# Performance work log

Hardware: AMD Instinct MI355X
Metric: run time of the kernel (lower is better)

Reference implementation:

```python
import jax, jax.numpy as jnp
import numpy as np

B, S, D, H, DFF = 4, 2048, 512, 8, 2048
HD = D // H  # head dim = 64
LN_EPS = 1e-5


def setup_inputs() -> dict:
    key = jax.random.key(0)
    ks = jax.random.split(key, 12)
    sc = 0.02
    return {
        "x": jax.random.normal(ks[0], (B, S, D), jnp.float32),
        "Wq": jax.random.normal(ks[1], (D, D), jnp.float32) * sc,
        "bq": jnp.zeros((D,), jnp.float32),
        "Wk": jax.random.normal(ks[2], (D, D), jnp.float32) * sc,
        "bk": jnp.zeros((D,), jnp.float32),
        "Wv": jax.random.normal(ks[3], (D, D), jnp.float32) * sc,
        "bv": jnp.zeros((D,), jnp.float32),
        "W1": jax.random.normal(ks[4], (D, DFF), jnp.float32) * sc,
        "b1": jnp.zeros((DFF,), jnp.float32),
        "W2": jax.random.normal(ks[5], (DFF, D), jnp.float32) * sc,
        "b2": jnp.zeros((D,), jnp.float32),
        "gamma": jnp.ones((D,), jnp.float32),
        "beta": jnp.zeros((D,), jnp.float32),
    }


def reference(x, Wq, bq, Wk, bk, Wv, bv, W1, b1, W2, b2, gamma, beta):
    # Multi-head self-attention (explicit bmm -> softmax -> bmm chain)
    q = (x @ Wq + bq).reshape(B, S, H, HD)
    k = (x @ Wk + bk).reshape(B, S, H, HD)
    v = (x @ Wv + bv).reshape(B, S, H, HD)
    scores = jnp.einsum("bqhd,bkhd->bhqk", q, k) / jnp.sqrt(jnp.float32(HD))
    atn = jax.nn.softmax(scores, axis=-1)          # [B,H,S,S]
    attn_out = jnp.einsum("bhqk,bkhd->bqhd", atn, v).reshape(B, S, D)
    # FFN with residual + LayerNorm (residual around FFN only, as in source)
    h = jax.nn.relu(attn_out @ W1 + b1)
    y = h @ W2 + b2 + attn_out
    mu = jnp.mean(y, axis=-1, keepdims=True)
    var = jnp.var(y, axis=-1, keepdims=True)
    out = (y - mu) * jax.lax.rsqrt(var + LN_EPS) * gamma + beta
    return (out, atn)
```

## Files before the change

kernel.cpp:

```cpp
#include <hip/hip_runtime.h>
#include <hip/hip_bf16.h>

#define TPB 256
typedef long long ll;


using short8  = __attribute__((ext_vector_type(8))) short;
using short4v = __attribute__((ext_vector_type(4))) short;
using floatx4 = __attribute__((ext_vector_type(4))) float;

__device__ __forceinline__ unsigned short f2bu(float f) {
    union { float f; unsigned int u; } v; v.f = f;
    unsigned int u = v.u;
    return (unsigned short)((u + 0x7fffu + ((u >> 16) & 1u)) >> 16);
}

__device__ __forceinline__ float bu2f(unsigned short us) {
    union { unsigned int u; float f; } v; v.u = ((unsigned int)us) << 16;
    return v.f;
}

__device__ __forceinline__ unsigned int cvtpk(float lo, float hi) {
    unsigned int r;
    asm volatile("v_cvt_pk_bf16_f32 %0, %1, %2" : "=v"(r) : "v"(lo), "v"(hi));
    return r;
}

__device__ __forceinline__ float fexp2(float x) {
#if __has_builtin(__builtin_amdgcn_exp2f)
    return __builtin_amdgcn_exp2f(x);
#else
    float r;
    asm("v_exp_f32 %0, %1" : "=v"(r) : "v"(x));
    return r;
#endif
}

__device__ __forceinline__ floatx4 mfma16(short4v a, short4v b, floatx4 c) {
#if __has_builtin(__builtin_amdgcn_mfma_f32_16x16x16bf16_1k)
    return __builtin_amdgcn_mfma_f32_16x16x16bf16_1k(a, b, c, 0, 0, 0);
#else
    floatx4 d;
    asm volatile("v_mfma_f32_16x16x16_bf16 %0, %1, %2, %3"
                 : "=v"(d) : "v"(a), "v"(b), "v"(c));
    return d;
#endif
}

__device__ __forceinline__ void gload16(const unsigned short* g, unsigned short* l) {
    __builtin_amdgcn_global_load_lds(
        (const __attribute__((address_space(1))) void*)g,
        (__attribute__((address_space(3))) void*)l, 16, 0, 0);
}

#define QSCALE 0.18033688f

template<int BM, int BN, int EPI>
__device__ __forceinline__ void gemm_body(
    const unsigned short* __restrict__ Ap, const unsigned short* __restrict__ BTp,
    const float* __restrict__ bias, void* __restrict__ Cp,
    const unsigned short* __restrict__ Rb, unsigned short* __restrict__ Vtp,
    int K, ll lda, ll ldb, ll ldc, int bx, int by,
    unsigned short* Asm, unsigned short* Bsm)
{
    constexpr int BK = 64;
    const int tid  = threadIdx.x;
    const int lane = tid & 63;
    const int wave = tid >> 6;
    const int wm = wave >> 1, wn = wave & 1;
    constexpr int WM = BM / 2, WN = BN / 2, FM = WM / 16, FN = WN / 16;

    const ll brow = (ll)bx * BM;
    const ll bcol = (ll)by * BN;
    const int srow = lane >> 3;
    const int ssw  = (((lane & 7) ^ srow)) << 3;
    const int kswz = (lane & 7) << 3;

    floatx4 acc[FM][FN] = {};

    for (int k0 = 0; k0 < K; k0 += BK) {
        #pragma unroll
        for (int ii = 0; ii < BM / 32; ++ii) {
            int i = wave + ii * 4;
            gload16(Ap + (brow + i * 8 + srow) * lda + k0 + ssw, Asm + i * 512);
        }
        #pragma unroll
        for (int ii = 0; ii < BN / 32; ++ii) {
            int i = wave + ii * 4;
            gload16(BTp + (bcol + i * 8 + srow) * ldb + k0 + ssw, Bsm + i * 512);
        }
        __syncthreads();

        #pragma unroll
        for (int kk = 0; kk < BK; kk += 32) {
            short8 af[FM], bfr[FN];
            const int kidx = (kk + ((lane >> 4) << 3)) ^ kswz;
            const int ar = wm * WM + (lane & 15);
            const int bc = wn * WN + (lane & 15);
            #pragma unroll
            for (int m = 0; m < FM; m++)
                af[m] = *(const short8*)&Asm[(ar + m * 16) * BK + kidx];
            #pragma unroll
            for (int n = 0; n < FN; n++)
                bfr[n] = *(const short8*)&Bsm[(bc + n * 16) * BK + kidx];
            #pragma unroll
            for (int m = 0; m < FM; m++)
                #pragma unroll
                for (int n = 0; n < FN; n++)
                    acc[m][n] = __builtin_amdgcn_mfma_f32_16x16x32_bf16(af[m], bfr[n], acc[m][n], 0, 0, 0);
        }
        __syncthreads();
    }

    const ll crow0 = brow + wm * WM + ((lane >> 4) << 2);
    const ll ccol0 = bcol + wn * WN + (lane & 15);

    if constexpr (EPI == 7) {
        if (ccol0 >= 1024) {
            const int bz = (int)(brow >> 11);
            #pragma unroll
            for (int m = 0; m < FM; m++) {
                const int sl = (int)((crow0 + m * 16) & 2047);
                #pragma unroll
                for (int n = 0; n < FN; n++) {
                    const int col = (int)(ccol0 + n * 16);
                    const float bv = bias[col];
                    const int hdg = col - 1024;
                    unsigned int u0 = cvtpk(acc[m][n][0] + bv, acc[m][n][1] + bv);
                    unsigned int u1 = cvtpk(acc[m][n][2] + bv, acc[m][n][3] + bv);
                    int2 t = { (int)u0, (int)u1 };
                    *(int2*)(Vtp + ((ll)((bz * 8 + (hdg >> 6)) * 64 + (hdg & 63))) * 2048 + sl) = t;
                }
            }
            return;
        }
    }

    #pragma unroll
    for (int m = 0; m < FM; m++) {
        #pragma unroll
        for (int j = 0; j < 4; j++) {
            ll row = crow0 + m * 16 + j;
            #pragma unroll
            for (int np = 0; np < FN; np += 2) {
                ll col0 = ccol0 + np * 16;
                ll col1 = col0 + 16;
                float v0 = acc[m][np][j]     + bias[col0];
                float v1 = acc[m][np + 1][j] + bias[col1];
                if constexpr (EPI == 3) {
                    v0 = v0 > 0.f ? v0 : 0.f;
                    v1 = v1 > 0.f ? v1 : 0.f;
                } else if constexpr (EPI == 6) {
                    v0 += bu2f(Rb[row * ldc + col0]);
                    v1 += bu2f(Rb[row * ldc + col1]);
                } else if constexpr (EPI == 7) {
                    if (col0 < 512) v0 *= QSCALE;
                    if (col1 < 512) v1 *= QSCALE;
                }
                unsigned int r = cvtpk(v0, v1);
                ((unsigned short*)Cp)[row * ldc + col0] = (unsigned short)r;
                ((unsigned short*)Cp)[row * ldc + col1] = (unsigned short)(r >> 16);
            }
        }
    }
}

template<int BM, int BN, int EPI>
__global__ __launch_bounds__(TPB) void gemm_k(
    const unsigned short* __restrict__ Ap, const unsigned short* __restrict__ BTp,
    const float* __restrict__ bias, void* __restrict__ Cp,
    const unsigned short* __restrict__ Rb, unsigned short* __restrict__ Vtp,
    int K, ll lda, ll ldb, ll ldc)
{
    __shared__ unsigned short sh[BM * 64 + BN * 64];
    int nwg = gridDim.x * gridDim.y;
    int sid = blockIdx.y * gridDim.x + blockIdx.x;
    int cpx = nwg >> 3;
    int w = (sid & 7) * cpx + (sid >> 3);
    int bx = w % gridDim.x, by = w / gridDim.x;
    gemm_body<BM, BN, EPI>(Ap, BTp, bias, Cp, Rb, Vtp, K, lda, ldb, ldc, bx, by,
                           sh, sh + BM * 64);
}

__device__ __forceinline__ void atnwrite_body(
    const unsigned short* __restrict__ qkv, const float* __restrict__ ilbuf,
    float* __restrict__ atn, int bh, int qt, unsigned short* sh)
{
    unsigned short* Qsm = sh;
    unsigned short* Ksm = sh + 8192;
    float* Pst = (float*)sh;

    const int tid = threadIdx.x, lane = tid & 63, wave = tid >> 6;
    const int c0 = lane & 15, g = lane >> 4;
    const int b = bh >> 3, h = bh & 7;

    const ll qbase  = ((ll)(b * 2048 + qt * 128)) * 1536 + h * 64;
    const ll kbase0 = ((ll)(b * 2048)) * 1536 + 512 + h * 64;
    const int srow = lane >> 3;
    const int ssw  = (((lane & 7) ^ srow)) << 3;
    const int kswz = (lane & 7) << 3;

    #pragma unroll
    for (int ii = 0; ii < 4; ++ii) {
        int i = wave + ii * 4;
        gload16(qkv + qbase + (ll)(i * 8 + srow) * 1536 + ssw, Qsm + i * 512);
    }
    __syncthreads();
    short8 qf[2][2];
    #pragma unroll
    for (int nq = 0; nq < 2; nq++)
        #pragma unroll
        for (int kk = 0; kk < 2; kk++)
            qf[nq][kk] = *(const short8*)&Qsm[(wave * 32 + nq * 16 + c0) * 64 + ((kk * 32 + g * 8) ^ kswz)];

    float il2[2];
    #pragma unroll
    for (int nq = 0; nq < 2; nq++)
        il2[nq] = ilbuf[(ll)bh * 2048 + qt * 128 + wave * 32 + nq * 16 + c0];

    float* myP = Pst + wave * 1024;

    for (int kb = 0; kb < 16; ++kb) {
        const ll koff = kbase0 + (ll)kb * 128 * 1536;
        #pragma unroll
        for (int ii = 0; ii < 4; ++ii) {
            int i = wave + ii * 4;
            gload16(qkv + koff + (ll)(i * 8 + srow) * 1536 + ssw, Ksm + i * 512);
        }
        __syncthreads();

        floatx4 sacc[8][2] = {};
        #pragma unroll
        for (int kk = 0; kk < 2; kk++)
            #pragma unroll
            for (int mk = 0; mk < 8; mk++) {
                short8 kf = *(const short8*)&Ksm[(mk * 16 + c0) * 64 + ((kk * 32 + g * 8) ^ kswz)];
                #pragma unroll
                for (int nq = 0; nq < 2; nq++)
                    sacc[mk][nq] = __builtin_amdgcn_mfma_f32_16x16x32_bf16(kf, qf[nq][kk], sacc[mk][nq], 0, 0, 0);
            }

        #pragma unroll
        for (int mk = 0; mk < 8; mk++)
            #pragma unroll
            for (int nq = 0; nq < 2; nq++)
                #pragma unroll
                for (int r = 0; r < 4; r++)
                    sacc[mk][nq][r] = fexp2(sacc[mk][nq][r]) * il2[nq];

        #pragma unroll
        for (int nq = 0; nq < 2; nq++) {
            #pragma unroll
            for (int hf = 0; hf < 2; hf++) {
                if ((c0 >> 3) == hf) {
                    int rho = c0 & 7;
                    #pragma unroll
                    for (int mk = 0; mk < 8; mk++) {
                        int k4 = mk * 4 + g;
                        ((floatx4*)myP)[rho * 32 + (k4 ^ rho)] = sacc[mk][nq];
                    }
                }
                const ll grow = (ll)bh * 2048 + qt * 128 + wave * 32 + nq * 16 + hf * 8;
                #pragma unroll
                for (int t = 0; t < 4; t++) {
                    int rr = t * 2 + (lane >> 5);
                    int k4r = lane & 31;
                    floatx4 v = ((const floatx4*)myP)[rr * 32 + (k4r ^ rr)];
                    __builtin_nontemporal_store(
                        v, (floatx4*)(atn + (grow + rr) * 2048 + kb * 128 + k4r * 4));
                }
            }
        }
        __syncthreads();
    }
}

__global__ __launch_bounds__(512) void attn8_k(
    const unsigned short* __restrict__ qkv, const unsigned short* __restrict__ vt,
    unsigned short* __restrict__ attnb, float* __restrict__ ilbuf)
{
    __shared__ unsigned short sh[32768];

    const int tid = threadIdx.x, lane = tid & 63, w = tid >> 6;
    const int c0 = lane & 15, g = lane >> 4;
    const int srow = lane >> 3;
    const int ssw  = (((lane & 7) ^ srow)) << 3;
    const int kswz = (lane & 7) << 3;

    const int n = blockIdx.x;
    const int j = n >> 3;
    const int bh = (n & 7) * 4 + (j & 3);
    const int qp = j >> 2;
    const int b = bh >> 3, h = bh & 7;

    const ll qbase  = ((ll)(b * 2048 + qp * 256)) * 1536 + h * 64;
    const ll kbase0 = ((ll)(b * 2048)) * 1536 + 512 + h * 64;
    const unsigned short* vbase = vt + (ll)bh * 64 * 2048;

    #pragma unroll
    for (int ii = 0; ii < 4; ++ii) {
        int i = w + ii * 8;
        gload16(qkv + qbase + (ll)(i * 8 + srow) * 1536 + ssw, sh + i * 512);
    }
    __syncthreads();
    short8 qf[2][2];
    #pragma unroll
    for (int nq = 0; nq < 2; nq++)
        #pragma unroll
        for (int kk = 0; kk < 2; kk++)
            qf[nq][kk] = *(const short8*)&sh[(w * 32 + nq * 16 + c0) * 64 + ((kk * 32 + g * 8) ^ kswz)];
    __syncthreads();

    floatx4 oaccT[4][2] = {};
    float l_run[2] = {0.f, 0.f};

#define STAGE_KV(kbx, bb) do {                                                   \
    const ll koff_ = kbase0 + (ll)(kbx) * 128 * 1536;                            \
    unsigned short* Kd_ = sh + ((bb) << 13);                                     \
    unsigned short* Vd_ = sh + 16384 + ((bb) << 13);                             \
    _Pragma("unroll")                                                            \
    for (int ii = 0; ii < 2; ++ii) { int i = w + ii * 8;                         \
        gload16(qkv + koff_ + (ll)(i * 8 + srow) * 1536 + ssw, Kd_ + i * 512); } \
    _Pragma("unroll")                                                            \
    for (int ii = 0; ii < 2; ++ii) { int i = w + ii * 8; int s = i * 8 + srow;   \
        int vrow = s >> 1; int vslot = ((s & 1) << 3) | (lane & 7);              \
        gload16(vbase + (ll)vrow * 2048 + (kbx) * 128 + ((vslot ^ (vrow & 7)) << 3), \
                Vd_ + i * 512); }                                                \
} while (0)

    STAGE_KV(0, 0);
    for (int kb = 0; kb < 16; ++kb) {
        const int cur = kb & 1;
        if (kb < 15) {
            STAGE_KV(kb + 1, cur ^ 1);
            asm volatile("s_waitcnt vmcnt(4)" ::: "memory");
        } else {
            asm volatile("s_waitcnt vmcnt(0)" ::: "memory");
        }
        __builtin_amdgcn_sched_barrier(0);
        __builtin_amdgcn_s_barrier();
        __builtin_amdgcn_sched_barrier(0);

        unsigned short* Kc = sh + (cur << 13);
        unsigned short* Vc = sh + 16384 + (cur << 13);

        floatx4 sacc[8][2] = {};
        #pragma unroll
        for (int kk = 0; kk < 2; kk++)
            #pragma unroll
            for (int mk = 0; mk < 8; mk++) {
                short8 kf = *(const short8*)&Kc[(mk * 16 + c0) * 64 + ((kk * 32 + g * 8) ^ kswz)];
                #pragma unroll
                for (int nq = 0; nq < 2; nq++)
                    sacc[mk][nq] = __builtin_amdgcn_mfma_f32_16x16x32_bf16(kf, qf[nq][kk], sacc[mk][nq], 0, 0, 0);
            }

        #pragma unroll
        for (int nq = 0; nq < 2; nq++) {
            float rs = 0.f;
            #pragma unroll
            for (int mk = 0; mk < 8; mk++)
                #pragma unroll
                for (int r = 0; r < 4; r++) {
                    float p = fexp2(sacc[mk][nq][r]);
                    sacc[mk][nq][r] = p;
                    rs += p;
                }
            rs += __shfl_xor(rs, 16);
            rs += __shfl_xor(rs, 32);
            l_run[nq] += rs;
        }

        #pragma unroll
        for (int mk = 0; mk < 8; mk++) {
            short4v pb[2];
            #pragma unroll
            for (int nq = 0; nq < 2; nq++) {
                union { unsigned int u[2]; short4v s; } pu;
                pu.u[0] = cvtpk(sacc[mk][nq][0], sacc[mk][nq][1]);
                pu.u[1] = cvtpk(sacc[mk][nq][2], sacc[mk][nq][3]);
                pb[nq] = pu.s;
            }
            #pragma unroll
            for (int mk2 = 0; mk2 < 4; mk2++) {
                short4v vf = *(const short4v*)&Vc[(mk2 * 16 + c0) * 128 + ((mk * 16 + g * 4) ^ kswz)];
                #pragma unroll
                for (int nq = 0; nq < 2; nq++)
                    oaccT[mk2][nq] = mfma16(vf, pb[nq], oaccT[mk2][nq]);
            }
        }
        __builtin_amdgcn_sched_barrier(0);
        __builtin_amdgcn_s_barrier();
        __builtin_amdgcn_sched_barrier(0);
    }
#undef STAGE_KV

    const float il[2] = { 1.0f / l_run[0], 1.0f / l_run[1] };

    #pragma unroll
    for (int nq = 0; nq < 2; nq++) {
        int qrow = qp * 256 + w * 32 + nq * 16 + c0;
        ll row = (ll)b * 2048 + qrow;
        #pragma unroll
        for (int mk2 = 0; mk2 < 4; mk2++) {
            int col = h * 64 + mk2 * 16 + g * 4;
            unsigned int r0 = cvtpk(oaccT[mk2][nq][0] * il[nq], oaccT[mk2][nq][1] * il[nq]);
            unsigned int r1 = cvtpk(oaccT[mk2][nq][2] * il[nq], oaccT[mk2][nq][3] * il[nq]);
            int2 tb = { (int)r0, (int)r1 };
            *(int2*)&attnb[row * 512 + col] = tb;
        }
        if (g == 0) ilbuf[(ll)bh * 2048 + qrow] = il[nq];
    }
}

template<int WRBH0, int WRCNT, int GX, int GY, int BM, int BN, int EPI>
__global__ __launch_bounds__(TPB) void fusedg_k(
    const unsigned short* __restrict__ qkv, const float* __restrict__ ilbuf,
    float* __restrict__ atn,
    const unsigned short* __restrict__ Ap, const unsigned short* __restrict__ BTp,
    const float* __restrict__ bias, void* __restrict__ Cp,
    const unsigned short* __restrict__ Rb,
    int K, ll lda, ll ldb, ll ldc)
{
    __shared__ unsigned short sh[16384];
    const int bid = blockIdx.x;
    constexpr int WRN = WRCNT * 16;
    if (bid < WRN) {
        atnwrite_body(qkv, ilbuf, atn, WRBH0 + bid % WRCNT, bid / WRCNT, sh);
    } else {
        int sid = bid - WRN;
        constexpr int NWG = GX * GY;
        int w = (sid & 7) * (NWG >> 3) + (sid >> 3);
        int bx = w % GX, by = w / GX;
        gemm_body<BM, BN, EPI>(Ap, BTp, bias, Cp, Rb, nullptr, K, lda, ldb, ldc,
                               bx, by, sh, sh + BM * 64);
    }
}

__global__ __launch_bounds__(TPB) void ln_k(const unsigned short* __restrict__ y,
                                            const float* __restrict__ gamma,
                                            const float* __restrict__ beta,
                                            float* __restrict__ out)
{
    const int lane = threadIdx.x & 63;
    const ll row = (ll)blockIdx.x * 4 + (threadIdx.x >> 6);
    short8 v = *(const short8*)(y + row * 512 + lane * 8);
    float f[8];
    float s = 0.f, q = 0.f;
    #pragma unroll
    for (int j = 0; j < 8; j++) {
        f[j] = bu2f((unsigned short)v[j]);
        s += f[j]; q += f[j] * f[j];
    }
    #pragma unroll
    for (int off = 32; off; off >>= 1) { s += __shfl_xor(s, off); q += __shfl_xor(q, off); }
    const float mu  = s * (1.0f / 512.0f);
    const float var = q * (1.0f / 512.0f) - mu * mu;
    const float rs  = rsqrtf(var + 1e-5f);

    float4 g0 = *(const float4*)(gamma + lane * 8);
    float4 g1 = *(const float4*)(gamma + lane * 8 + 4);
    float4 e0 = *(const float4*)(beta  + lane * 8);
    float4 e1 = *(const float4*)(beta  + lane * 8 + 4);
    floatx4 o0, o1;
    o0[0] = (f[0] - mu) * rs * g0.x + e0.x;  o0[1] = (f[1] - mu) * rs * g0.y + e0.y;
    o0[2] = (f[2] - mu) * rs * g0.z + e0.z;  o0[3] = (f[3] - mu) * rs * g0.w + e0.w;
    o1[0] = (f[4] - mu) * rs * g1.x + e1.x;  o1[1] = (f[5] - mu) * rs * g1.y + e1.y;
    o1[2] = (f[6] - mu) * rs * g1.z + e1.z;  o1[3] = (f[7] - mu) * rs * g1.w + e1.w;
    __builtin_nontemporal_store(o0, (floatx4*)(out + row * 512 + lane * 8));
    __builtin_nontemporal_store(o1, (floatx4*)(out + row * 512 + lane * 8 + 4));
}

__global__ __launch_bounds__(TPB) void prep_k(
    const float* __restrict__ Wq, const float* __restrict__ Wk,
    const float* __restrict__ Wv, const float* __restrict__ W1,
    const float* __restrict__ W2,
    const float* __restrict__ bq, const float* __restrict__ bk,
    const float* __restrict__ bv, const float* __restrict__ x,
    unsigned short* __restrict__ wtqkv, unsigned short* __restrict__ wt1,
    unsigned short* __restrict__ wt2, float* __restrict__ bqkv,
    unsigned short* __restrict__ xb)
{
    __shared__ float t[32 * 33];
    const int bid = blockIdx.x;
    const float* W; unsigned short* WT; int K, N, tile;
    if (bid < 256)       { W = Wq; WT = wtqkv;             K = 512;  N = 512;  tile = bid; }
    else if (bid < 512)  { W = Wk; WT = wtqkv + 512 * 512; K = 512;  N = 512;  tile = bid - 256; }
    else if (bid < 768)  { W = Wv; WT = wtqkv + 1024 * 512;K = 512;  N = 512;  tile = bid - 512; }
    else if (bid < 1792) { W = W1; WT = wt1;               K = 512;  N = 2048; tile = bid - 768; }
    else if (bid < 2816) { W = W2; WT = wt2;               K = 2048; N = 512;  tile = bid - 1792; }
    else if (bid < 2822) {
        int i = (bid - 2816) * TPB + threadIdx.x;
        if (i < 512)       bqkv[i] = bq[i];
        else if (i < 1024) bqkv[i] = bk[i - 512];
        else if (i < 1536) bqkv[i] = bv[i - 1024];
        return;
    } else {
        ll i = ((ll)(bid - 2822) * TPB + threadIdx.x) * 4;
        float4 v = *(const float4*)(x + i);
        unsigned int r0 = cvtpk(v.x, v.y), r1 = cvtpk(v.z, v.w);
        int2 tt = { (int)r0, (int)r1 };
        *(int2*)(xb + i) = tt;
        return;
    }
    const int nx = N >> 5;
    const int n0 = (tile % nx) * 32, k0 = (tile / nx) * 32;
    const int tx = threadIdx.x & 31, ty = threadIdx.x >> 5;
    #pragma unroll
    for (int i = ty; i < 32; i += 8) t[i * 33 + tx] = W[(ll)(k0 + i) * N + n0 + tx];
    __syncthreads();
    #pragma unroll
    for (int i = ty; i < 32; i += 8) WT[(ll)(n0 + i) * K + k0 + tx] = f2bu(t[tx * 33 + i]);
}

extern "C" void kernel_launch(void* const* d_in, const int* in_sizes, int n_in,
                              void* d_out, int out_size, void* d_ws, size_t ws_size,
                              hipStream_t stream)
{
    (void)in_sizes; (void)n_in; (void)out_size; (void)ws_size;
    const float* x     = (const float*)d_in[0];
    const float* Wq    = (const float*)d_in[1];
    const float* bq    = (const float*)d_in[2];
    const float* Wk    = (const float*)d_in[3];
    const float* bk    = (const float*)d_in[4];
    const float* Wv    = (const float*)d_in[5];
    const float* bv    = (const float*)d_in[6];
    const float* W1    = (const float*)d_in[7];
    const float* b1    = (const float*)d_in[8];
    const float* W2    = (const float*)d_in[9];
    const float* b2    = (const float*)d_in[10];
    const float* gamma = (const float*)d_in[11];
    const float* beta  = (const float*)d_in[12];

    char* ws = (char*)d_ws;
    size_t off = 0;
    auto alloc = [&](size_t bytes) -> char* {
        char* p = ws + off; off += (bytes + 255) & ~(size_t)255; return p;
    };
    unsigned short* xb    = (unsigned short*)alloc(8192ll * 512 * 2);
    unsigned short* wtqkv = (unsigned short*)alloc(1536ll * 512 * 2);
    unsigned short* wt1   = (unsigned short*)alloc(2048ll * 512 * 2);
    unsigned short* wt2   = (unsigned short*)alloc(512ll * 2048 * 2);
    float*          bqkv  = (float*)alloc(1536 * 4);
    unsigned short* qkv   = (unsigned short*)alloc(8192ll * 1536 * 2);
    unsigned short* vt    = (unsigned short*)alloc(32ll * 64 * 2048 * 2);
    unsigned short* attnb = (unsigned short*)alloc(8192ll * 512 * 2);
    unsigned short* hmid  = (unsigned short*)alloc(8192ll * 2048 * 2);
    unsigned short* ybuf  = (unsigned short*)alloc(8192ll * 512 * 2);
    float*          ilbuf = (float*)alloc(32ll * 2048 * 4);

    float* outp = (float*)d_out;
    float* atn  = outp + 4194304;

    prep_k<<<2822 + 4096, TPB, 0, stream>>>(Wq, Wk, Wv, W1, W2, bq, bk, bv, x,
                                            wtqkv, wt1, wt2, bqkv, xb);

    gemm_k<128, 128, 7><<<dim3(64, 12, 1), TPB, 0, stream>>>(
        xb, wtqkv, bqkv, qkv, nullptr, vt, 512, 512, 512, 1536);

    attn8_k<<<256, 512, 0, stream>>>(qkv, vt, attnb, ilbuf);

    fusedg_k<0, 16, 64, 16, 128, 128, 3><<<256 + 1024, TPB, 0, stream>>>(
        qkv, ilbuf, atn,
        attnb, wt1, b1, hmid, nullptr, 512, 512, 512, 2048);

    fusedg_k<16, 16, 128, 4, 64, 128, 6><<<256 + 512, TPB, 0, stream>>>(
        qkv, ilbuf, atn,
        hmid, wt2, b2, ybuf, attnb, 2048, 2048, 2048, 512);

    ln_k<<<2048, TPB, 0, stream>>>(ybuf, gamma, beta, outp);
}
```

Baseline: 260.1 us.

## Merge attention and attn-matrix writers into one kernel, recompute softmax denominators locally

New measurement: 344.6 us. +32.5%, slower.

```diff
diff --git a/kernel.cpp b/kernel.cpp
--- a/kernel.cpp
+++ b/kernel.cpp
@@ -182,9 +182,9 @@
                            sh, sh + BM * 64);
 }
 
-__device__ __forceinline__ void atnwrite_body(
-    const unsigned short* __restrict__ qkv, const float* __restrict__ ilbuf,
-    float* __restrict__ atn, int bh, int qt, unsigned short* sh)
+__device__ __forceinline__ void wr4_body(
+    const unsigned short* __restrict__ qkv, float* __restrict__ atn,
+    int bh, int qt, unsigned short* sh)
 {
     unsigned short* Qsm = sh;
     unsigned short* Ksm = sh + 8192;
@@ -212,11 +212,44 @@
         #pragma unroll
         for (int kk = 0; kk < 2; kk++)
             qf[nq][kk] = *(const short8*)&Qsm[(wave * 32 + nq * 16 + c0) * 64 + ((kk * 32 + g * 8) ^ kswz)];
-
-    float il2[2];
-    #pragma unroll
-    for (int nq = 0; nq < 2; nq++)
-        il2[nq] = ilbuf[(ll)bh * 2048 + qt * 128 + wave * 32 + nq * 16 + c0];
+    __syncthreads();
+
+    float l_run[2] = {0.f, 0.f};
+    for (int kb = 0; kb < 16; ++kb) {
+        const ll koff = kbase0 + (ll)kb * 128 * 1536;
+        #pragma unroll
+        for (int ii = 0; ii < 4; ++ii) {
+            int i = wave + ii * 4;
+            gload16(qkv + koff + (ll)(i * 8 + srow) * 1536 + ssw, Ksm + i * 512);
+        }
+        __syncthreads();
+
+        floatx4 sacc[8][2] = {};
+        #pragma unroll
+        for (int kk = 0; kk < 2; kk++)
+            #pragma unroll
+            for (int mk = 0; mk < 8; mk++) {
+                short8 kf = *(const short8*)&Ksm[(mk * 16 + c0) * 64 + ((kk * 32 + g * 8) ^ kswz)];
+                #pragma unroll
+                for (int nq = 0; nq < 2; nq++)
+                    sacc[mk][nq] = __builtin_amdgcn_mfma_f32_16x16x32_bf16(kf, qf[nq][kk], sacc[mk][nq], 0, 0, 0);
+            }
+
+        #pragma unroll
+        for (int nq = 0; nq < 2; nq++) {
+            float rs = 0.f;
+            #pragma unroll
+            for (int mk = 0; mk < 8; mk++)
+                #pragma unroll
+                for (int r = 0; r < 4; r++)
+                    rs += fexp2(sacc[mk][nq][r]);
+            rs += __shfl_xor(rs, 16);
+            rs += __shfl_xor(rs, 32);
+            l_run[nq] += rs;
+        }
+        __syncthreads();
+    }
+    const float il2[2] = { 1.0f / l_run[0], 1.0f / l_run[1] };
 
     float* myP = Pst + wave * 1024;
 
@@ -275,31 +308,24 @@
     }
 }
 
-__global__ __launch_bounds__(512) void attn8_k(
+__device__ __forceinline__ void attn4_body(
     const unsigned short* __restrict__ qkv, const unsigned short* __restrict__ vt,
-    unsigned short* __restrict__ attnb, float* __restrict__ ilbuf)
-{
-    __shared__ unsigned short sh[32768];
-
-    const int tid = threadIdx.x, lane = tid & 63, w = tid >> 6;
+    unsigned short* __restrict__ attnb, int bh, int qt, unsigned short* sh)
+{
+    const int tid = threadIdx.x, lane = tid & 63, wave = tid >> 6;
     const int c0 = lane & 15, g = lane >> 4;
     const int srow = lane >> 3;
     const int ssw  = (((lane & 7) ^ srow)) << 3;
     const int kswz = (lane & 7) << 3;
-
-    const int n = blockIdx.x;
-    const int j = n >> 3;
-    const int bh = (n & 7) * 4 + (j & 3);
-    const int qp = j >> 2;
     const int b = bh >> 3, h = bh & 7;
 
-    const ll qbase  = ((ll)(b * 2048 + qp * 256)) * 1536 + h * 64;
+    const ll qbase  = ((ll)(b * 2048 + qt * 128)) * 1536 + h * 64;
     const ll kbase0 = ((ll)(b * 2048)) * 1536 + 512 + h * 64;
     const unsigned short* vbase = vt + (ll)bh * 64 * 2048;
 
     #pragma unroll
     for (int ii = 0; ii < 4; ++ii) {
-        int i = w + ii * 8;
+        int i = wave + ii * 4;
         gload16(qkv + qbase + (ll)(i * 8 + srow) * 1536 + ssw, sh + i * 512);
     }
     __syncthreads();
@@ -308,7 +334,7 @@
     for (int nq = 0; nq < 2; nq++)
         #pragma unroll
         for (int kk = 0; kk < 2; kk++)
-            qf[nq][kk] = *(const short8*)&sh[(w * 32 + nq * 16 + c0) * 64 + ((kk * 32 + g * 8) ^ kswz)];
+            qf[nq][kk] = *(const short8*)&sh[(wave * 32 + nq * 16 + c0) * 64 + ((kk * 32 + g * 8) ^ kswz)];
     __syncthreads();
 
     floatx4 oaccT[4][2] = {};
@@ -319,10 +345,10 @@
     unsigned short* Kd_ = sh + ((bb) << 13);                                     \
     unsigned short* Vd_ = sh + 16384 + ((bb) << 13);                             \
     _Pragma("unroll")                                                            \
-    for (int ii = 0; ii < 2; ++ii) { int i = w + ii * 8;                         \
+    for (int ii = 0; ii < 4; ++ii) { int i = wave + ii * 4;                      \
         gload16(qkv + koff_ + (ll)(i * 8 + srow) * 1536 + ssw, Kd_ + i * 512); } \
     _Pragma("unroll")                                                            \
-    for (int ii = 0; ii < 2; ++ii) { int i = w + ii * 8; int s = i * 8 + srow;   \
+    for (int ii = 0; ii < 4; ++ii) { int i = wave + ii * 4; int s = i * 8 + srow;\
         int vrow = s >> 1; int vslot = ((s & 1) << 3) | (lane & 7);              \
         gload16(vbase + (ll)vrow * 2048 + (kbx) * 128 + ((vslot ^ (vrow & 7)) << 3), \
                 Vd_ + i * 512); }                                                \
@@ -333,7 +359,7 @@
         const int cur = kb & 1;
         if (kb < 15) {
             STAGE_KV(kb + 1, cur ^ 1);
-            asm volatile("s_waitcnt vmcnt(4)" ::: "memory");
+            asm volatile("s_waitcnt vmcnt(8)" ::: "memory");
         } else {
             asm volatile("s_waitcnt vmcnt(0)" ::: "memory");
         }
@@ -399,7 +425,7 @@
 
     #pragma unroll
     for (int nq = 0; nq < 2; nq++) {
-        int qrow = qp * 256 + w * 32 + nq * 16 + c0;
+        int qrow = qt * 128 + wave * 32 + nq * 16 + c0;
         ll row = (ll)b * 2048 + qrow;
         #pragma unroll
         for (int mk2 = 0; mk2 < 4; mk2++) {
@@ -409,14 +435,28 @@
             int2 tb = { (int)r0, (int)r1 };
             *(int2*)&attnb[row * 512 + col] = tb;
         }
-        if (g == 0) ilbuf[(ll)bh * 2048 + qrow] = il[nq];
-    }
-}
-
-template<int WRBH0, int WRCNT, int GX, int GY, int BM, int BN, int EPI>
+    }
+}
+
+__global__ __launch_bounds__(TPB) void mega_k(
+    const unsigned short* __restrict__ qkv, const unsigned short* __restrict__ vt,
+    unsigned short* __restrict__ attnb, float* __restrict__ atn)
+{
+    __shared__ unsigned short sh[32768];
+    const int bid = blockIdx.x;
+    if (bid < 512) {
+        const int xcd = bid & 7, j = bid >> 3;
+        attn4_body(qkv, vt, attnb, xcd * 4 + (j & 3), j >> 2, sh);
+    } else {
+        const int m = bid - 512;
+        const int xcd = m & 7, j = m >> 3;
+        wr4_body(qkv, atn, xcd * 4 + (j % 3), j / 3, sh);
+    }
+}
+
+template<int QT0, int GX, int GY, int BM, int BN, int EPI>
 __global__ __launch_bounds__(TPB) void fusedg_k(
-    const unsigned short* __restrict__ qkv, const float* __restrict__ ilbuf,
-    float* __restrict__ atn,
+    const unsigned short* __restrict__ qkv, float* __restrict__ atn,
     const unsigned short* __restrict__ Ap, const unsigned short* __restrict__ BTp,
     const float* __restrict__ bias, void* __restrict__ Cp,
     const unsigned short* __restrict__ Rb,
@@ -424,11 +464,11 @@
 {
     __shared__ unsigned short sh[16384];
     const int bid = blockIdx.x;
-    constexpr int WRN = WRCNT * 16;
-    if (bid < WRN) {
-        atnwrite_body(qkv, ilbuf, atn, WRBH0 + bid % WRCNT, bid / WRCNT, sh);
+    if (bid < 64) {
+        const int xcd = bid & 7, qt = QT0 + (bid >> 3);
+        wr4_body(qkv, atn, xcd * 4 + 3, qt, sh);
     } else {
-        int sid = bid - WRN;
+        int sid = bid - 64;
         constexpr int NWG = GX * GY;
         int w = (sid & 7) * (NWG >> 3) + (sid >> 3);
         int bx = w % GX, by = w / GX;
@@ -547,7 +587,6 @@
     unsigned short* attnb = (unsigned short*)alloc(8192ll * 512 * 2);
     unsigned short* hmid  = (unsigned short*)alloc(8192ll * 2048 * 2);
     unsigned short* ybuf  = (unsigned short*)alloc(8192ll * 512 * 2);
-    float*          ilbuf = (float*)alloc(32ll * 2048 * 4);
 
     float* outp = (float*)d_out;
     float* atn  = outp + 4194304;
@@ -558,14 +597,14 @@
     gemm_k<128, 128, 7><<<dim3(64, 12, 1), TPB, 0, stream>>>(
         xb, wtqkv, bqkv, qkv, nullptr, vt, 512, 512, 512, 1536);
 
-    attn8_k<<<256, 512, 0, stream>>>(qkv, vt, attnb, ilbuf);
-
-    fusedg_k<0, 16, 64, 16, 128, 128, 3><<<256 + 1024, TPB, 0, stream>>>(
-        qkv, ilbuf, atn,
+    mega_k<<<896, TPB, 0, stream>>>(qkv, vt, attnb, atn);
+
+    fusedg_k<0, 64, 16, 128, 128, 3><<<64 + 1024, TPB, 0, stream>>>(
+        qkv, atn,
         attnb, wt1, b1, hmid, nullptr, 512, 512, 512, 2048);
 
-    fusedg_k<16, 16, 128, 4, 64, 128, 6><<<256 + 512, TPB, 0, stream>>>(
-        qkv, ilbuf, atn,
+    fusedg_k<8, 128, 4, 64, 128, 6><<<64 + 512, TPB, 0, stream>>>(
+        qkv, atn,
         hmid, wt2, b2, ybuf, attnb, 2048, 2048, 2048, 512);
 
     ln_k<<<2048, TPB, 0, stream>>>(ybuf, gamma, beta, outp);
```
